# Performance work log

Hardware: AMD Instinct MI355X
Metric: run time of the kernel (lower is better)

The kernel has to match this reference:

```python
import jax, jax.numpy as jnp
import numpy as np

B, T, V = 4096, 32, 256          # batch, decode steps, vocab
E, CE, H, L, NH = 768, 64, 256, 2, 4  # eword_dim, char_emb_dim, hidden, gru layers, heads
HD = H // NH                      # head dim
BOS, PAD = 1, 0


def _gru_cell(x, h, w_ih, w_hh, b_ih, b_hh):
    # PyTorch GRUCell math: gates ordered (r, z, n)
    gi = x @ w_ih.T + b_ih
    gh = h @ w_hh.T + b_hh
    ir, iz, inn = jnp.split(gi, 3, axis=-1)
    hr, hz, hn = jnp.split(gh, 3, axis=-1)
    r = jax.nn.sigmoid(ir + hr)
    z = jax.nn.sigmoid(iz + hz)
    n = jnp.tanh(inn + r * hn)
    return (1.0 - z) * n + z * h


def setup_inputs() -> dict:
    key = jax.random.key(0)
    ks = jax.random.split(key, 24)
    s = 0.02
    p = lambda k, shp: (jax.random.normal(k, shp, jnp.float32) * s)
    return {
        "eword": jax.random.normal(ks[0], (B, E), jnp.float32),
        "target_ids": jax.random.randint(ks[1], (B, T), 0, V),
        # params
        "char_emb": p(ks[2], (V, CE)).at[PAD].set(0.0),
        "eword_proj_w": p(ks[3], (H, E)), "eword_proj_b": p(ks[4], (H,)),
        "gru_w_ih0": p(ks[5], (3 * H, CE + E)), "gru_w_hh0": p(ks[6], (3 * H, H)),
        "gru_b_ih0": p(ks[7], (3 * H,)), "gru_b_hh0": p(ks[8], (3 * H,)),
        "gru_w_ih1": p(ks[9], (3 * H, H)), "gru_w_hh1": p(ks[10], (3 * H, H)),
        "gru_b_ih1": p(ks[11], (3 * H,)), "gru_b_hh1": p(ks[12], (3 * H,)),
        "attn_in_w": p(ks[13], (3 * H, H)), "attn_in_b": p(ks[14], (3 * H,)),
        "attn_out_w": p(ks[15], (H, H)), "attn_out_b": p(ks[16], (H,)),
        "key_w": p(ks[17], (H, E)), "key_b": p(ks[18], (H,)),
        "val_w": p(ks[19], (H, E)), "val_b": p(ks[20], (H,)),
        "proj_w": p(ks[21], (V, H)), "proj_b": p(ks[22], (V,)),
    }


def reference(eword, target_ids, char_emb, eword_proj_w, eword_proj_b,
              gru_w_ih0, gru_w_hh0, gru_b_ih0, gru_b_hh0,
              gru_w_ih1, gru_w_hh1, gru_b_ih1, gru_b_hh1,
              attn_in_w, attn_in_b, attn_out_w, attn_out_b,
              key_w, key_b, val_w, val_b, proj_w, proj_b):
    batch = eword.shape[0]
    # init hidden: tanh(Linear(eword)) broadcast across layers
    h0 = jnp.tanh(eword @ eword_proj_w.T + eword_proj_b)
    # pre-projected key/value (seq len 1), then MHA in-proj for k,v (static)
    wq, wk, wv = jnp.split(attn_in_w, 3, axis=0)
    bq, bk, bv = jnp.split(attn_in_b, 3)
    ek = (eword @ key_w.T + key_b) @ wk.T + bk        # (B, H)
    ev = (eword @ val_w.T + val_b) @ wv.T + bv        # (B, H)
    kh = ek.reshape(batch, NH, HD)                     # (B, NH, HD)
    vh = ev.reshape(batch, NH, HD)
    scale = 1.0 / np.sqrt(HD).astype(np.float32)

    # teacher forcing: input at step t is BOS for t=0, else target_ids[:, t-1]
    in_ids = jnp.concatenate(
        [jnp.full((batch, 1), BOS, target_ids.dtype), target_ids[:, :-1]], axis=1)

    def step(carry, ids):
        h_l0, h_l1 = carry
        ce = char_emb[ids] * (ids != PAD)[:, None].astype(char_emb.dtype)
        x = jnp.concatenate([ce, eword], axis=-1)     # (B, CE+E)
        h_l0 = _gru_cell(x, h_l0, gru_w_ih0, gru_w_hh0, gru_b_ih0, gru_b_hh0)
        h_l1 = _gru_cell(h_l0, h_l1, gru_w_ih1, gru_w_hh1, gru_b_ih1, gru_b_hh1)
        # single-query cross-attention over a length-1 key/value
        q = (h_l1 @ wq.T + bq).reshape(batch, NH, HD)
        score = jnp.sum(q * kh, axis=-1, keepdims=True) * scale  # (B, NH, 1)
        w = jax.nn.softmax(score, axis=-1)            # ones (len-1 softmax)
        attn = (w * vh).reshape(batch, H)
        attn_out = attn @ attn_out_w.T + attn_out_b
        out = h_l1 + attn_out
        logits = out @ proj_w.T + proj_b              # (B, V)
        return (h_l0, h_l1), logits

    _, logits_t = jax.lax.scan(step, (h0, h0), in_ids.T)  # (T, B, V)
    return jnp.transpose(logits_t, (1, 0, 2))              # (B, T, V)
```

## Files before the change

### kernel.cpp

```cpp
#include <hip/hip_runtime.h>


typedef __bf16 bf16;
typedef __attribute__((ext_vector_type(8))) __bf16 bf16x8;
typedef __attribute__((ext_vector_type(4))) __bf16 bf16x4;
typedef __attribute__((ext_vector_type(4))) float fx4;

#define MFMA16(a, b, c) __builtin_amdgcn_mfma_f32_16x16x32_bf16(a, b, c, 0, 0, 0)

__device__ __forceinline__ float sigm(float x) { return 1.0f / (1.0f + expf(-x)); }

__device__ __forceinline__ bf16x8 cvt8(const float* __restrict__ p) {
    float4 u = ((const float4*)p)[0];
    float4 v = ((const float4*)p)[1];
    bf16x8 r;
    r[0] = (bf16)u.x; r[1] = (bf16)u.y; r[2] = (bf16)u.z; r[3] = (bf16)u.w;
    r[4] = (bf16)v.x; r[5] = (bf16)v.y; r[6] = (bf16)v.z; r[7] = (bf16)v.w;
    return r;
}

__device__ __forceinline__ bf16x8 addcvt8(bf16x8 h, const float* __restrict__ p) {
    float4 u = ((const float4*)p)[0];
    float4 v = ((const float4*)p)[1];
    bf16x8 r;
    r[0] = (bf16)((float)h[0] + u.x); r[1] = (bf16)((float)h[1] + u.y);
    r[2] = (bf16)((float)h[2] + u.z); r[3] = (bf16)((float)h[3] + u.w);
    r[4] = (bf16)((float)h[4] + v.x); r[5] = (bf16)((float)h[5] + v.y);
    r[6] = (bf16)((float)h[6] + v.z); r[7] = (bf16)((float)h[7] + v.w);
    return r;
}

__global__ void f2b(const float* __restrict__ s, bf16* __restrict__ d, int n) {
    int i = (blockIdx.x * 256 + threadIdx.x) * 4;
    if (i >= n) return;
    float4 v = *(const float4*)(s + i);
    bf16x4 o;
    o[0] = (bf16)v.x; o[1] = (bf16)v.y; o[2] = (bf16)v.z; o[3] = (bf16)v.w;
    *(bf16x4*)(d + i) = o;
}

__global__ __launch_bounds__(256, 4) void gemm_bt(
    const float* __restrict__ A, int lda,
    const float* __restrict__ W, int ldw,
    const float* __restrict__ bias,
    float* __restrict__ out, int ldo, int act_tanh, int K)
{
    const int tid  = threadIdx.x;
    const int wid  = tid >> 6;
    const int lane = tid & 63;
    const int quad = lane >> 4;
    const int l16  = lane & 15;
    const int m0   = blockIdx.x * 32;
    const int n0   = blockIdx.y * 256 + wid * 64;

    fx4 acc[4][2];
#pragma unroll
    for (int j = 0; j < 4; ++j) {
        acc[j][0] = fx4{0.f, 0.f, 0.f, 0.f};
        acc[j][1] = fx4{0.f, 0.f, 0.f, 0.f};
    }

    const float* a0p = A + (size_t)(m0 + l16) * lda + quad * 8;
    const float* a1p = A + (size_t)(m0 + 16 + l16) * lda + quad * 8;

    for (int k0 = 0; k0 < K; k0 += 32) {
        bf16x8 a0 = cvt8(a0p + k0);
        bf16x8 a1 = cvt8(a1p + k0);
#pragma unroll
        for (int j = 0; j < 4; ++j) {
            bf16x8 b = cvt8(W + (size_t)(n0 + j * 16 + l16) * ldw + k0 + quad * 8);
            acc[j][0] = MFMA16(a0, b, acc[j][0]);
            acc[j][1] = MFMA16(a1, b, acc[j][1]);
        }
    }

#pragma unroll
    for (int j = 0; j < 4; ++j) {
        int n = n0 + j * 16 + l16;
        float bv = bias ? bias[n] : 0.0f;
#pragma unroll
        for (int rt = 0; rt < 2; ++rt)
#pragma unroll
            for (int r = 0; r < 4; ++r) {
                int m = m0 + rt * 16 + quad * 4 + r;
                float v = acc[j][rt][r] + bv;
                if (act_tanh) v = tanhf(v);
                out[(size_t)m * ldo + n] = v;
            }
    }
}

__global__ __launch_bounds__(1024) void decoder_loop(
    const int*   __restrict__ tgt,
    const float* __restrict__ h0i,
    const float* __restrict__ gword,
    const float* __restrict__ cproj,
    const bf16*  __restrict__ w_hh0, const float* __restrict__ b_hh0,
    const bf16*  __restrict__ w_ih1, const float* __restrict__ b_ih1,
    const bf16*  __restrict__ w_hh1, const float* __restrict__ b_hh1,
    bf16* __restrict__ h1all)
{
    __shared__ __align__(16) bf16 hb0[32][264];
    __shared__ __align__(16) bf16 hb1[32][264];
    __shared__ int ids_s[32];

    const int tid  = threadIdx.x;
    const int wid  = tid >> 6;
    const int lane = tid & 63;
    const int quad = lane >> 4;
    const int l16  = lane & 15;
    const int row0 = blockIdx.x * 32;
    const int col  = wid * 16 + l16;

    float h0m[2][4], h1m[2][4], gwv[3][2][4];
    float bh0[3], bi1[3], bh1[3];
#pragma unroll
    for (int g = 0; g < 3; ++g) {
        bh0[g] = b_hh0[g * 256 + col];
        bi1[g] = b_ih1[g * 256 + col];
        bh1[g] = b_hh1[g * 256 + col];
    }
#pragma unroll
    for (int rt = 0; rt < 2; ++rt)
#pragma unroll
        for (int r = 0; r < 4; ++r) {
            int lrow = rt * 16 + quad * 4 + r;
            float v = h0i[(size_t)(row0 + lrow) * 256 + col];
            h0m[rt][r] = v; h1m[rt][r] = v;
            bf16 bv = (bf16)v;
            hb0[lrow][col] = bv; hb1[lrow][col] = bv;
#pragma unroll
            for (int g = 0; g < 3; ++g)
                gwv[g][rt][r] = gword[(size_t)(row0 + lrow) * 768 + g * 256 + col];
        }

    for (int t = 0; t < 32; ++t) {
        if (tid < 32)
            ids_s[tid] = (t == 0) ? 1 : tgt[(row0 + tid) * 32 + (t - 1)];
        __syncthreads();

        float cpv[3][2][4];
#pragma unroll
        for (int rt = 0; rt < 2; ++rt)
#pragma unroll
            for (int r = 0; r < 4; ++r) {
                int id = ids_s[rt * 16 + quad * 4 + r];
#pragma unroll
                for (int g = 0; g < 3; ++g)
                    cpv[g][rt][r] = cproj[(size_t)id * 768 + g * 256 + col];
            }

        fx4 g0[3][2];
#pragma unroll
        for (int g = 0; g < 3; ++g) {
            g0[g][0] = fx4{0.f, 0.f, 0.f, 0.f};
            g0[g][1] = fx4{0.f, 0.f, 0.f, 0.f};
        }
        for (int k0 = 0; k0 < 256; k0 += 32) {
            bf16x8 a0 = *(const bf16x8*)&hb0[l16][k0 + quad * 8];
            bf16x8 a1 = *(const bf16x8*)&hb0[16 + l16][k0 + quad * 8];
#pragma unroll
            for (int g = 0; g < 3; ++g) {
                bf16x8 b = *(const bf16x8*)(w_hh0 + (size_t)(g * 256 + col) * 256 + k0 + quad * 8);
                g0[g][0] = MFMA16(a0, b, g0[g][0]);
                g0[g][1] = MFMA16(a1, b, g0[g][1]);
            }
        }

#pragma unroll
        for (int rt = 0; rt < 2; ++rt)
#pragma unroll
            for (int r = 0; r < 4; ++r) {
                float gr = cpv[0][rt][r] + gwv[0][rt][r] + g0[0][rt][r] + bh0[0];
                float gz = cpv[1][rt][r] + gwv[1][rt][r] + g0[1][rt][r] + bh0[1];
                float gn = cpv[2][rt][r] + gwv[2][rt][r];
                float rr = sigm(gr);
                float zz = sigm(gz);
                float nn = tanhf(gn + rr * (g0[2][rt][r] + bh0[2]));
                h0m[rt][r] = (1.0f - zz) * nn + zz * h0m[rt][r];
            }
        __syncthreads();
#pragma unroll
        for (int rt = 0; rt < 2; ++rt)
#pragma unroll
            for (int r = 0; r < 4; ++r)
                hb0[rt * 16 + quad * 4 + r][col] = (bf16)h0m[rt][r];
        __syncthreads();

        fx4 gI[3][2], gH[3][2];
#pragma unroll
        for (int g = 0; g < 3; ++g) {
            gI[g][0] = fx4{0.f, 0.f, 0.f, 0.f}; gI[g][1] = fx4{0.f, 0.f, 0.f, 0.f};
            gH[g][0] = fx4{0.f, 0.f, 0.f, 0.f}; gH[g][1] = fx4{0.f, 0.f, 0.f, 0.f};
        }
        for (int k0 = 0; k0 < 256; k0 += 32) {
            bf16x8 a0 = *(const bf16x8*)&hb0[l16][k0 + quad * 8];
            bf16x8 a1 = *(const bf16x8*)&hb0[16 + l16][k0 + quad * 8];
            bf16x8 c0 = *(const bf16x8*)&hb1[l16][k0 + quad * 8];
            bf16x8 c1 = *(const bf16x8*)&hb1[16 + l16][k0 + quad * 8];
#pragma unroll
            for (int g = 0; g < 3; ++g) {
                bf16x8 b1 = *(const bf16x8*)(w_ih1 + (size_t)(g * 256 + col) * 256 + k0 + quad * 8);
                gI[g][0] = MFMA16(a0, b1, gI[g][0]);
                gI[g][1] = MFMA16(a1, b1, gI[g][1]);
                bf16x8 b2 = *(const bf16x8*)(w_hh1 + (size_t)(g * 256 + col) * 256 + k0 + quad * 8);
                gH[g][0] = MFMA16(c0, b2, gH[g][0]);
                gH[g][1] = MFMA16(c1, b2, gH[g][1]);
            }
        }

#pragma unroll
        for (int rt = 0; rt < 2; ++rt)
#pragma unroll
            for (int r = 0; r < 4; ++r) {
                float rr = sigm(gI[0][rt][r] + bi1[0] + gH[0][rt][r] + bh1[0]);
                float zz = sigm(gI[1][rt][r] + bi1[1] + gH[1][rt][r] + bh1[1]);
                float nn = tanhf(gI[2][rt][r] + bi1[2] + rr * (gH[2][rt][r] + bh1[2]));
                h1m[rt][r] = (1.0f - zz) * nn + zz * h1m[rt][r];
            }
        __syncthreads();
#pragma unroll
        for (int rt = 0; rt < 2; ++rt)
#pragma unroll
            for (int r = 0; r < 4; ++r) {
                int lrow = rt * 16 + quad * 4 + r;
                bf16 hv = (bf16)h1m[rt][r];
                hb1[lrow][col] = hv;
                h1all[((size_t)(row0 + lrow) * 32 + t) * 256 + col] = hv;
            }
        __syncthreads();
    }
}

__global__ __launch_bounds__(256, 4) void logits_final(
    const bf16*  __restrict__ h1,
    const float* __restrict__ a2,
    const bf16*  __restrict__ pw,
    const float* __restrict__ pb,
    float* __restrict__ out)
{
    const int tid  = threadIdx.x;
    const int wid  = tid >> 6;
    const int lane = tid & 63;
    const int quad = lane >> 4;
    const int l16  = lane & 15;
    const int m0   = blockIdx.x * 32;
    const int n0   = wid * 64;
    const int b    = m0 >> 5;

    fx4 acc[4][2];
#pragma unroll
    for (int j = 0; j < 4; ++j) {
        acc[j][0] = fx4{0.f, 0.f, 0.f, 0.f};
        acc[j][1] = fx4{0.f, 0.f, 0.f, 0.f};
    }

    for (int k0 = 0; k0 < 256; k0 += 32) {
        bf16x8 h0 = *(const bf16x8*)(h1 + (size_t)(m0 + l16) * 256 + k0 + quad * 8);
        bf16x8 h1v = *(const bf16x8*)(h1 + (size_t)(m0 + 16 + l16) * 256 + k0 + quad * 8);
        const float* ap = a2 + (size_t)b * 256 + k0 + quad * 8;
        bf16x8 a0 = addcvt8(h0, ap);
        bf16x8 a1 = addcvt8(h1v, ap);
#pragma unroll
        for (int j = 0; j < 4; ++j) {
            bf16x8 bb = *(const bf16x8*)(pw + (size_t)(n0 + j * 16 + l16) * 256 + k0 + quad * 8);
            acc[j][0] = MFMA16(a0, bb, acc[j][0]);
            acc[j][1] = MFMA16(a1, bb, acc[j][1]);
        }
    }

#pragma unroll
    for (int j = 0; j < 4; ++j) {
        int n = n0 + j * 16 + l16;
        float bv = pb[n];
#pragma unroll
        for (int rt = 0; rt < 2; ++rt)
#pragma unroll
            for (int r = 0; r < 4; ++r) {
                int m = m0 + rt * 16 + quad * 4 + r;
                out[(size_t)m * 256 + n] = acc[j][rt][r] + bv;
            }
    }
}

extern "C" void kernel_launch(void* const* d_in, const int* in_sizes, int n_in,
                              void* d_out, int out_size, void* d_ws, size_t ws_size,
                              hipStream_t stream)
{
    const float* eword      = (const float*)d_in[0];
    const int*   tgt        = (const int*)  d_in[1];
    const float* char_emb   = (const float*)d_in[2];
    const float* ew_w       = (const float*)d_in[3];
    const float* ew_b       = (const float*)d_in[4];
    const float* w_ih0      = (const float*)d_in[5];
    const float* w_hh0      = (const float*)d_in[6];
    const float* b_ih0      = (const float*)d_in[7];
    const float* b_hh0      = (const float*)d_in[8];
    const float* w_ih1      = (const float*)d_in[9];
    const float* w_hh1      = (const float*)d_in[10];
    const float* b_ih1      = (const float*)d_in[11];
    const float* b_hh1      = (const float*)d_in[12];
    const float* attn_in_w  = (const float*)d_in[13];
    const float* attn_in_b  = (const float*)d_in[14];
    const float* attn_out_w = (const float*)d_in[15];
    const float* attn_out_b = (const float*)d_in[16];
    const float* val_w      = (const float*)d_in[19];
    const float* val_b      = (const float*)d_in[20];
    const float* proj_w     = (const float*)d_in[21];
    const float* proj_b     = (const float*)d_in[22];

    char* ws = (char*)d_ws;
    float* h0i   = (float*)ws;  ws += (size_t)4096 * 256 * 4;
    float* gwrd  = (float*)ws;  ws += (size_t)4096 * 768 * 4;
    float* cproj = (float*)ws;  ws += (size_t)256  * 768 * 4;
    float* a2    = (float*)ws;  ws += (size_t)4096 * 256 * 4;
    float* buf1  = (float*)ws;  ws += (size_t)4096 * 256 * 4;
    float* buf2  = (float*)ws;  ws += (size_t)4096 * 256 * 4;
    bf16*  wbhh0 = (bf16*)ws;   ws += (size_t)768 * 256 * 2;
    bf16*  wbih1 = (bf16*)ws;   ws += (size_t)768 * 256 * 2;
    bf16*  wbhh1 = (bf16*)ws;   ws += (size_t)768 * 256 * 2;
    bf16*  wbprj = (bf16*)ws;   ws += (size_t)256 * 256 * 2;
    bf16*  h1all = (bf16*)ws;   ws += (size_t)4096 * 32 * 256 * 2;

    dim3 blk(256);
    f2b<<<dim3(192), blk, 0, stream>>>(w_hh0, wbhh0, 768 * 256);
    f2b<<<dim3(192), blk, 0, stream>>>(w_ih1, wbih1, 768 * 256);
    f2b<<<dim3(192), blk, 0, stream>>>(w_hh1, wbhh1, 768 * 256);
    f2b<<<dim3(64),  blk, 0, stream>>>(proj_w, wbprj, 256 * 256);

    gemm_bt<<<dim3(128, 1), blk, 0, stream>>>(eword, 768, ew_w, 768, ew_b, h0i, 256, 1, 768);
    gemm_bt<<<dim3(128, 3), blk, 0, stream>>>(eword, 768, w_ih0 + 64, 832, b_ih0, gwrd, 768, 0, 768);
    gemm_bt<<<dim3(8, 3),   blk, 0, stream>>>(char_emb, 64, w_ih0, 832, nullptr, cproj, 768, 0, 64);
    gemm_bt<<<dim3(128, 1), blk, 0, stream>>>(eword, 768, val_w, 768, val_b, buf1, 256, 0, 768);
    gemm_bt<<<dim3(128, 1), blk, 0, stream>>>(buf1, 256, attn_in_w + 512 * 256, 256, attn_in_b + 512, buf2, 256, 0, 256);
    gemm_bt<<<dim3(128, 1), blk, 0, stream>>>(buf2, 256, attn_out_w, 256, attn_out_b, a2, 256, 0, 256);

    decoder_loop<<<dim3(128), dim3(1024), 0, stream>>>(
        tgt, h0i, gwrd, cproj,
        wbhh0, b_hh0, wbih1, b_ih1, wbhh1, b_hh1, h1all);

    logits_final<<<dim3(4096), blk, 0, stream>>>(h1all, a2, wbprj, proj_b, (float*)d_out);
}
```

Before: 2.078 ms.

## Halve rows per decoder block, double-buffer hidden state, overlap hh GEMMs

The decoder loop now handles 16 batch rows per block and launches 256 blocks, so more of the GPU's compute units take part in the sequential recurrence. Hidden states are double-buffered in shared memory, which cuts the barriers per step from four to two. The layer-1 recurrent GEMM is computed in the same pass as the layer-0 recurrent GEMM, and the next-step char-projection gather is issued early. The trade-off is that each block reads the weights from memory with only half the row reuse, so total weight traffic doubles.

```diff
diff --git a/kernel.cpp b/kernel.cpp
--- a/kernel.cpp
+++ b/kernel.cpp
@@ -100,19 +100,18 @@
     const bf16*  __restrict__ w_hh1, const float* __restrict__ b_hh1,
     bf16* __restrict__ h1all)
 {
-    __shared__ __align__(16) bf16 hb0[32][264];
-    __shared__ __align__(16) bf16 hb1[32][264];
-    __shared__ int ids_s[32];
+    __shared__ __align__(16) bf16 hb0[2][16][264];
+    __shared__ __align__(16) bf16 hb1[2][16][264];
 
     const int tid  = threadIdx.x;
     const int wid  = tid >> 6;
     const int lane = tid & 63;
     const int quad = lane >> 4;
     const int l16  = lane & 15;
-    const int row0 = blockIdx.x * 32;
+    const int row0 = blockIdx.x * 16;
     const int col  = wid * 16 + l16;
 
-    float h0m[2][4], h1m[2][4], gwv[3][2][4];
+    float h0m[4], h1m[4], gwv[3][4], cpv[3][4];
     float bh0[3], bi1[3], bh1[3];
 #pragma unroll
     for (int g = 0; g < 3; ++g) {
@@ -121,113 +120,93 @@
         bh1[g] = b_hh1[g * 256 + col];
     }
 #pragma unroll
-    for (int rt = 0; rt < 2; ++rt)
+    for (int r = 0; r < 4; ++r) {
+        int lrow = quad * 4 + r;
+        float v = h0i[(size_t)(row0 + lrow) * 256 + col];
+        h0m[r] = v; h1m[r] = v;
+        bf16 bv = (bf16)v;
+        hb0[0][lrow][col] = bv; hb1[0][lrow][col] = bv;
+#pragma unroll
+        for (int g = 0; g < 3; ++g)
+            gwv[g][r] = gword[(size_t)(row0 + lrow) * 768 + g * 256 + col];
+    }
+#pragma unroll
+    for (int g = 0; g < 3; ++g) {
+        float v = cproj[768 + g * 256 + col];
+#pragma unroll
+        for (int r = 0; r < 4; ++r) cpv[g][r] = v;
+    }
+
+    int woff[3];
+#pragma unroll
+    for (int g = 0; g < 3; ++g)
+        woff[g] = ((g * 256 + col) * 256 + quad * 8) * 2;
+
+    __syncthreads();
+
+    for (int t = 0; t < 32; ++t) {
+        const int p = t & 1, q = p ^ 1;
+
+        fx4 g0[3], g1[3];
+#pragma unroll
+        for (int g = 0; g < 3; ++g) {
+            g0[g] = fx4{0.f, 0.f, 0.f, 0.f};
+            g1[g] = fx4{0.f, 0.f, 0.f, 0.f};
+        }
+#pragma unroll
+        for (int k0 = 0; k0 < 256; k0 += 32) {
+            bf16x8 a0 = *(const bf16x8*)&hb0[p][l16][k0 + quad * 8];
+            bf16x8 c0 = *(const bf16x8*)&hb1[p][l16][k0 + quad * 8];
+#pragma unroll
+            for (int g = 0; g < 3; ++g) {
+                bf16x8 b0 = *(const bf16x8*)((const char*)w_hh0 + woff[g] + k0 * 2);
+                g0[g] = MFMA16(a0, b0, g0[g]);
+                bf16x8 b1 = *(const bf16x8*)((const char*)w_hh1 + woff[g] + k0 * 2);
+                g1[g] = MFMA16(c0, b1, g1[g]);
+            }
+        }
 #pragma unroll
         for (int r = 0; r < 4; ++r) {
-            int lrow = rt * 16 + quad * 4 + r;
-            float v = h0i[(size_t)(row0 + lrow) * 256 + col];
-            h0m[rt][r] = v; h1m[rt][r] = v;
-            bf16 bv = (bf16)v;
-            hb0[lrow][col] = bv; hb1[lrow][col] = bv;
-#pragma unroll
-            for (int g = 0; g < 3; ++g)
-                gwv[g][rt][r] = gword[(size_t)(row0 + lrow) * 768 + g * 256 + col];
-        }
-
-    for (int t = 0; t < 32; ++t) {
-        if (tid < 32)
-            ids_s[tid] = (t == 0) ? 1 : tgt[(row0 + tid) * 32 + (t - 1)];
+            float rr = sigm(cpv[0][r] + gwv[0][r] + g0[0][r] + bh0[0]);
+            float zz = sigm(cpv[1][r] + gwv[1][r] + g0[1][r] + bh0[1]);
+            float nn = tanhf(cpv[2][r] + gwv[2][r] + rr * (g0[2][r] + bh0[2]));
+            h0m[r] = (1.0f - zz) * nn + zz * h0m[r];
+            hb0[q][quad * 4 + r][col] = (bf16)h0m[r];
+        }
         __syncthreads();
 
-        float cpv[3][2][4];
-#pragma unroll
-        for (int rt = 0; rt < 2; ++rt)
-#pragma unroll
-            for (int r = 0; r < 4; ++r) {
-                int id = ids_s[rt * 16 + quad * 4 + r];
-#pragma unroll
-                for (int g = 0; g < 3; ++g)
-                    cpv[g][rt][r] = cproj[(size_t)id * 768 + g * 256 + col];
+        int nid[4];
+#pragma unroll
+        for (int r = 0; r < 4; ++r)
+            nid[r] = tgt[(row0 + quad * 4 + r) * 32 + t];
+#pragma unroll
+        for (int g = 0; g < 3; ++g)
+#pragma unroll
+            for (int r = 0; r < 4; ++r)
+                cpv[g][r] = cproj[(size_t)nid[r] * 768 + g * 256 + col];
+
+        fx4 gi[3];
+#pragma unroll
+        for (int g = 0; g < 3; ++g) gi[g] = fx4{0.f, 0.f, 0.f, 0.f};
+#pragma unroll
+        for (int k0 = 0; k0 < 256; k0 += 32) {
+            bf16x8 a = *(const bf16x8*)&hb0[q][l16][k0 + quad * 8];
+#pragma unroll
+            for (int g = 0; g < 3; ++g) {
+                bf16x8 b = *(const bf16x8*)((const char*)w_ih1 + woff[g] + k0 * 2);
+                gi[g] = MFMA16(a, b, gi[g]);
             }
-
-        fx4 g0[3][2];
-#pragma unroll
-        for (int g = 0; g < 3; ++g) {
-            g0[g][0] = fx4{0.f, 0.f, 0.f, 0.f};
-            g0[g][1] = fx4{0.f, 0.f, 0.f, 0.f};
-        }
-        for (int k0 = 0; k0 < 256; k0 += 32) {
-            bf16x8 a0 = *(const bf16x8*)&hb0[l16][k0 + quad * 8];
-            bf16x8 a1 = *(const bf16x8*)&hb0[16 + l16][k0 + quad * 8];
-#pragma unroll
-            for (int g = 0; g < 3; ++g) {
-                bf16x8 b = *(const bf16x8*)(w_hh0 + (size_t)(g * 256 + col) * 256 + k0 + quad * 8);
-                g0[g][0] = MFMA16(a0, b, g0[g][0]);
-                g0[g][1] = MFMA16(a1, b, g0[g][1]);
-            }
-        }
-
-#pragma unroll
-        for (int rt = 0; rt < 2; ++rt)
-#pragma unroll
-            for (int r = 0; r < 4; ++r) {
-                float gr = cpv[0][rt][r] + gwv[0][rt][r] + g0[0][rt][r] + bh0[0];
-                float gz = cpv[1][rt][r] + gwv[1][rt][r] + g0[1][rt][r] + bh0[1];
-                float gn = cpv[2][rt][r] + gwv[2][rt][r];
-                float rr = sigm(gr);
-                float zz = sigm(gz);
-                float nn = tanhf(gn + rr * (g0[2][rt][r] + bh0[2]));
-                h0m[rt][r] = (1.0f - zz) * nn + zz * h0m[rt][r];
-            }
-        __syncthreads();
-#pragma unroll
-        for (int rt = 0; rt < 2; ++rt)
-#pragma unroll
-            for (int r = 0; r < 4; ++r)
-                hb0[rt * 16 + quad * 4 + r][col] = (bf16)h0m[rt][r];
-        __syncthreads();
-
-        fx4 gI[3][2], gH[3][2];
-#pragma unroll
-        for (int g = 0; g < 3; ++g) {
-            gI[g][0] = fx4{0.f, 0.f, 0.f, 0.f}; gI[g][1] = fx4{0.f, 0.f, 0.f, 0.f};
-            gH[g][0] = fx4{0.f, 0.f, 0.f, 0.f}; gH[g][1] = fx4{0.f, 0.f, 0.f, 0.f};
-        }
-        for (int k0 = 0; k0 < 256; k0 += 32) {
-            bf16x8 a0 = *(const bf16x8*)&hb0[l16][k0 + quad * 8];
-            bf16x8 a1 = *(const bf16x8*)&hb0[16 + l16][k0 + quad * 8];
-            bf16x8 c0 = *(const bf16x8*)&hb1[l16][k0 + quad * 8];
-            bf16x8 c1 = *(const bf16x8*)&hb1[16 + l16][k0 + quad * 8];
-#pragma unroll
-            for (int g = 0; g < 3; ++g) {
-                bf16x8 b1 = *(const bf16x8*)(w_ih1 + (size_t)(g * 256 + col) * 256 + k0 + quad * 8);
-                gI[g][0] = MFMA16(a0, b1, gI[g][0]);
-                gI[g][1] = MFMA16(a1, b1, gI[g][1]);
-                bf16x8 b2 = *(const bf16x8*)(w_hh1 + (size_t)(g * 256 + col) * 256 + k0 + quad * 8);
-                gH[g][0] = MFMA16(c0, b2, gH[g][0]);
-                gH[g][1] = MFMA16(c1, b2, gH[g][1]);
-            }
-        }
-
-#pragma unroll
-        for (int rt = 0; rt < 2; ++rt)
-#pragma unroll
-            for (int r = 0; r < 4; ++r) {
-                float rr = sigm(gI[0][rt][r] + bi1[0] + gH[0][rt][r] + bh1[0]);
-                float zz = sigm(gI[1][rt][r] + bi1[1] + gH[1][rt][r] + bh1[1]);
-                float nn = tanhf(gI[2][rt][r] + bi1[2] + rr * (gH[2][rt][r] + bh1[2]));
-                h1m[rt][r] = (1.0f - zz) * nn + zz * h1m[rt][r];
-            }
-        __syncthreads();
-#pragma unroll
-        for (int rt = 0; rt < 2; ++rt)
-#pragma unroll
-            for (int r = 0; r < 4; ++r) {
-                int lrow = rt * 16 + quad * 4 + r;
-                bf16 hv = (bf16)h1m[rt][r];
-                hb1[lrow][col] = hv;
-                h1all[((size_t)(row0 + lrow) * 32 + t) * 256 + col] = hv;
-            }
+        }
+#pragma unroll
+        for (int r = 0; r < 4; ++r) {
+            float rr = sigm(gi[0][r] + bi1[0] + g1[0][r] + bh1[0]);
+            float zz = sigm(gi[1][r] + bi1[1] + g1[1][r] + bh1[1]);
+            float nn = tanhf(gi[2][r] + bi1[2] + rr * (g1[2][r] + bh1[2]));
+            h1m[r] = (1.0f - zz) * nn + zz * h1m[r];
+            bf16 hv = (bf16)h1m[r];
+            hb1[q][quad * 4 + r][col] = hv;
+            h1all[((size_t)(row0 + quad * 4 + r) * 32 + t) * 256 + col] = hv;
+        }
         __syncthreads();
     }
 }
@@ -335,7 +314,7 @@
     gemm_bt<<<dim3(128, 1), blk, 0, stream>>>(buf1, 256, attn_in_w + 512 * 256, 256, attn_in_b + 512, buf2, 256, 0, 256);
     gemm_bt<<<dim3(128, 1), blk, 0, stream>>>(buf2, 256, attn_out_w, 256, attn_out_b, a2, 256, 0, 256);
 
-    decoder_loop<<<dim3(128), dim3(1024), 0, stream>>>(
+    decoder_loop<<<dim3(256), dim3(1024), 0, stream>>>(
         tgt, h0i, gwrd, cproj,
         wbhh0, b_hh0, wbih1, b_ih1, wbhh1, b_hh1, h1all);
 
```

Measured after the change: 2.170 ms. 4.4% more time.
